# Kernel optimization log

Measured on AMD Instinct MI355X. Metric: run time of the kernel, lower is better.

The kernel has to match this reference:

```python
import jax, jax.numpy as jnp
import numpy as np

EPS_ATTN = 1e-6
EPS_LN = 1e-5  # torch nn.LayerNorm default eps
NHEAD = 8
L, D, DFF, S, B = 4, 512, 1024, 4096, 8


def _layernorm(x, g, b):
    m = jnp.mean(x, axis=-1, keepdims=True)
    v = jnp.mean((x - m) ** 2, axis=-1, keepdims=True)
    return (x - m) * jax.lax.rsqrt(v + EPS_LN) * g + b


def _layer(src, Wq, bq, Wk, bk, Wv, bv, Wo, bo, g1, be1, W1, bf1, W2, bf2, g2, be2):
    # src: (S, B, D)
    s, b, d = src.shape
    dk = d // NHEAD
    Q = (src @ Wq + bq).reshape(s, b, NHEAD, dk)
    K = (src @ Wk + bk).reshape(s, b, NHEAD, dk)
    V = (src @ Wv + bv).reshape(s, b, NHEAD, dk)
    # ELU+1 feature-map linear attention, vectorized over heads
    phiQ = jax.nn.elu(Q) + 1.0
    phiK = jax.nn.elu(K) + 1.0
    context = jnp.einsum('sbhd,sbhe->bhde', phiK, V)          # (B,H,dk,dk)
    out = jnp.einsum('sbhd,bhde->sbhe', phiQ, context)        # (S,B,H,dk)
    denom = jnp.einsum('sbhd,bhd->sbh', phiQ, phiK.sum(0))    # (S,B,H)
    out = out / (denom[..., None] + EPS_ATTN)
    attn = out.reshape(s, b, d)  # concat heads (same order as torch cat)
    out = attn @ Wo + bo
    out = _layernorm(src + out, g1, be1)
    ffn = jax.nn.relu(out @ W1 + bf1) @ W2 + bf2
    return _layernorm(out + ffn, g2, be2)


def setup_inputs() -> dict:
    key = jax.random.key(0)
    ks = jax.random.split(key, 8)
    sc = 0.02
    inp = {
        'src': jax.random.normal(ks[0], (S, B, D), jnp.float32),
        'Wq': jax.random.normal(ks[1], (L, D, D), jnp.float32) * sc,
        'bq': jnp.zeros((L, D), jnp.float32),
        'Wk': jax.random.normal(ks[2], (L, D, D), jnp.float32) * sc,
        'bk': jnp.zeros((L, D), jnp.float32),
        'Wv': jax.random.normal(ks[3], (L, D, D), jnp.float32) * sc,
        'bv': jnp.zeros((L, D), jnp.float32),
        'Wo': jax.random.normal(ks[4], (L, D, D), jnp.float32) * sc,
        'bo': jnp.zeros((L, D), jnp.float32),
        'ln1_g': jnp.ones((L, D), jnp.float32),
        'ln1_b': jnp.zeros((L, D), jnp.float32),
        'W1': jax.random.normal(ks[5], (L, D, DFF), jnp.float32) * sc,
        'b1': jnp.zeros((L, DFF), jnp.float32),
        'W2': jax.random.normal(ks[6], (L, DFF, D), jnp.float32) * sc,
        'b2': jnp.zeros((L, D), jnp.float32),
        'ln2_g': jnp.ones((L, D), jnp.float32),
        'ln2_b': jnp.zeros((L, D), jnp.float32),
    }
    return inp


def reference(src, Wq, bq, Wk, bk, Wv, bv, Wo, bo, ln1_g, ln1_b, W1, b1, W2, b2, ln2_g, ln2_b):
    x = src
    for i in range(Wq.shape[0]):  # small fixed layer count
        x = _layer(x, Wq[i], bq[i], Wk[i], bk[i], Wv[i], bv[i], Wo[i], bo[i],
                   ln1_g[i], ln1_b[i], W1[i], b1[i], W2[i], b2[i], ln2_g[i], ln2_b[i])
    return x
```

## Files before the change

kernel.cpp:

```cpp
#include <hip/hip_runtime.h>
#include <hip/hip_bf16.h>
#include <cstdint>

typedef __attribute__((ext_vector_type(8))) short short8;
typedef __attribute__((ext_vector_type(4))) float f32x4;
typedef __attribute__((ext_vector_type(4))) unsigned short ushort4v;

#define DEV static __device__ __forceinline__

DEV float bf2f(unsigned short u) {
    union { unsigned int i; float f; } v; v.i = ((unsigned int)u) << 16; return v.f;
}
DEV unsigned short f2bf(float f) {
    union { float f; unsigned int i; } v; v.f = f;
    unsigned int x = v.i;
    unsigned int r = x + 0x7fffu + ((x >> 16) & 1u);
    return (unsigned short)(r >> 16);
}

template<int EPI, int NBY, int LDA, int KT>
__global__ __launch_bounds__(256) void gemm_kernel(
    const unsigned short* __restrict__ A,
    const unsigned short* __restrict__ Bt,
    const float* __restrict__ bias,
    unsigned short* __restrict__ out1, int ldc1,
    unsigned short* __restrict__ out2)
{
    __shared__ unsigned short lds[128 * 136];
    const int t  = threadIdx.x;
    const int w  = t >> 6, l = t & 63;
    const int wr = w >> 1, wc = w & 1;
    const int lr = l & 15, lg = l >> 4;
    const int bid = blockIdx.x;
    const int j8  = bid & 7, s = bid >> 3;
    const int bx  = j8 * 32 + s / NBY;
    const int by  = s % NBY;
    const long tM = (long)bx * 128;
    const long tN = (long)by * 128;

    f32x4 acc[4][4];
#pragma unroll
    for (int i = 0; i < 4; i++)
#pragma unroll
        for (int j = 0; j < 4; j++) acc[i][j] = f32x4{0.f, 0.f, 0.f, 0.f};

    const unsigned short* ga[4];
    const unsigned short* gb[4];
    unsigned int ldsa[4], ldsb[4];
#pragma unroll
    for (int j = 0; j < 4; j++) {
        int c = (w * 4 + j) * 64 + l;
        int row = c >> 3, sc = (c & 7) ^ (row & 7);
        ga[j] = A + (tM + row) * LDA + sc * 8;
        gb[j] = Bt + (tN + row) * (long)KT + sc * 8;
        ldsa[j] = (w * 4 + j) * 512;
        ldsb[j] = 8192 + (w * 4 + j) * 512;
    }

#pragma unroll
    for (int kt = 0; kt < KT; kt += 64) {
#pragma unroll
        for (int j = 0; j < 4; j++)
            __builtin_amdgcn_global_load_lds(
                (const __attribute__((address_space(1))) void*)(ga[j] + kt),
                (__attribute__((address_space(3))) void*)(lds + ldsa[j]), 16, 0, 0);
#pragma unroll
        for (int j = 0; j < 4; j++)
            __builtin_amdgcn_global_load_lds(
                (const __attribute__((address_space(1))) void*)(gb[j] + kt),
                (__attribute__((address_space(3))) void*)(lds + ldsb[j]), 16, 0, 0);
        __syncthreads();
#pragma unroll
        for (int kk = 0; kk < 2; kk++) {
            short8 af[4], bfv[4];
#pragma unroll
            for (int mi = 0; mi < 4; mi++) {
                int r  = wr * 64 + mi * 16 + lr;
                int kc = kk * 4 + lg;
                af[mi] = *(const short8*)&lds[r * 64 + ((kc ^ (r & 7)) << 3)];
            }
#pragma unroll
            for (int ni = 0; ni < 4; ni++) {
                int n  = wc * 64 + ni * 16 + lr;
                int kc = kk * 4 + lg;
                bfv[ni] = *(const short8*)&lds[8192 + n * 64 + ((kc ^ (n & 7)) << 3)];
            }
#pragma unroll
            for (int mi = 0; mi < 4; mi++)
#pragma unroll
                for (int ni = 0; ni < 4; ni++)
                    acc[mi][ni] = __builtin_amdgcn_mfma_f32_16x16x32_bf16(
                        af[mi], bfv[ni], acc[mi][ni], 0, 0, 0);
        }
        __syncthreads();
    }

    float bv[4];
#pragma unroll
    for (int ni = 0; ni < 4; ni++) bv[ni] = bias[tN + wc * 64 + ni * 16 + lr];
    const bool doElu = (EPI == 0) && (tN < 512 || tN >= 1024);

#pragma unroll
    for (int mi = 0; mi < 4; mi++)
#pragma unroll
        for (int ni = 0; ni < 4; ni++)
#pragma unroll
            for (int j = 0; j < 4; j++) {
                float v = acc[mi][ni][j] + bv[ni];
                if (EPI == 0) { if (doElu) v = (v > 0.f) ? (v + 1.f) : expf(v); }
                if (EPI == 2) v = fmaxf(v, 0.f);
                int r = wr * 64 + mi * 16 + lg * 4 + j;
                int c = wc * 64 + ni * 16 + lr;
                lds[r * 136 + c] = f2bf(v);
            }
    __syncthreads();
    const bool toQ = (NBY == 12) && (tN >= 1024);
    unsigned short* o = toQ ? out2 : out1;
    const long ldc   = toQ ? 512 : ldc1;
    const long cb    = toQ ? (tN - 1024) : tN;
#pragma unroll
    for (int i = 0; i < 8; i++) {
        int q = i * 256 + t;
        int r = q >> 4, cc = q & 15;
        short8 v8 = *(const short8*)&lds[r * 136 + cc * 8];
        *(short8*)&o[(tM + r) * ldc + cb + cc * 8] = v8;
    }
}

template<int RESBF, int WRITEOF, int KT>
__global__ __launch_bounds__(512) void gemm_ln_kernel(
    const unsigned short* __restrict__ A, int lda,
    const unsigned short* __restrict__ Bt,
    const float* __restrict__ bias,
    const void* __restrict__ resp,
    const float* __restrict__ g,
    const float* __restrict__ be,
    float* __restrict__ of,
    unsigned short* __restrict__ ob,
    int unused)
{
    __shared__ unsigned short sA[2][128 * 32];
    __shared__ unsigned short sB[2][512 * 32];
    float* redb  = (float*)&sA[0][0];
    float* statb = redb + 1024;
    unsigned short* bb16 = (unsigned short*)&sB[0][0];
    const int t = threadIdx.x, w = t >> 6, l = t & 63, lr = l & 15, lg = l >> 4;
    const int wr = w >> 2, wc = w & 3;
    const long tM = (long)blockIdx.x * 128;

    f32x4 acc[4][8];
#pragma unroll
    for (int i = 0; i < 4; i++)
#pragma unroll
        for (int j = 0; j < 8; j++) acc[i][j] = f32x4{0.f, 0.f, 0.f, 0.f};

    const unsigned short* gA;
    const unsigned short* gB[4];
    unsigned int la, lb[4];
    {
        int c = t, row = c >> 2, sc = (c & 3) ^ ((row >> 1) & 3);
        gA = A + (tM + row) * (long)lda + sc * 8;
        la = (w * 64) * 8;
    }
#pragma unroll
    for (int j = 0; j < 4; j++) {
        int c = j * 512 + t, row = c >> 2, sc = (c & 3) ^ ((row >> 1) & 3);
        gB[j] = Bt + (long)row * KT + sc * 8;
        lb[j] = (j * 512 + w * 64) * 8;
    }

    auto STAGE = [&](int buf, int kt) {
        __builtin_amdgcn_global_load_lds(
            (const __attribute__((address_space(1))) void*)(gA + kt),
            (__attribute__((address_space(3))) void*)(&sA[buf][la]), 16, 0, 0);
#pragma unroll
        for (int j = 0; j < 4; j++)
            __builtin_amdgcn_global_load_lds(
                (const __attribute__((address_space(1))) void*)(gB[j] + kt),
                (__attribute__((address_space(3))) void*)(&sB[buf][lb[j]]), 16, 0, 0);
    };

    auto COMPUTE = [&](int buf) {
        short8 av[4], bw[8];
#pragma unroll
        for (int mi = 0; mi < 4; mi++) {
            int r = wr * 64 + mi * 16 + lr;
            av[mi] = *(const short8*)&sA[buf][r * 32 + ((lg ^ ((r >> 1) & 3)) << 3)];
        }
#pragma unroll
        for (int ni = 0; ni < 8; ni++) {
            int n = wc * 128 + ni * 16 + lr;
            bw[ni] = *(const short8*)&sB[buf][n * 32 + ((lg ^ ((n >> 1) & 3)) << 3)];
        }
#pragma unroll
        for (int mi = 0; mi < 4; mi++)
#pragma unroll
            for (int ni = 0; ni < 8; ni++)
                acc[mi][ni] = __builtin_amdgcn_mfma_f32_16x16x32_bf16(
                    av[mi], bw[ni], acc[mi][ni], 0, 0, 0);
    };

    STAGE(0, 0);
    STAGE(1, 32);
#pragma unroll
    for (int kt = 0; kt < KT; kt += 32) {
        if (kt < KT - 32) asm volatile("s_waitcnt vmcnt(5)" ::: "memory");
        else              asm volatile("s_waitcnt vmcnt(0)" ::: "memory");
        __builtin_amdgcn_s_barrier();
        COMPUTE((kt >> 5) & 1);
        asm volatile("s_waitcnt lgkmcnt(0)" ::: "memory");
        __builtin_amdgcn_s_barrier();
        if (kt + 64 < KT) STAGE((kt >> 5) & 1, kt + 64);
    }

    const float* resf = (const float*)resp;
    const unsigned short* resb = (const unsigned short*)resp;
    float gv[8], bev[8], bb[8];
#pragma unroll
    for (int ni = 0; ni < 8; ni++) {
        int col = wc * 128 + ni * 16 + lr;
        gv[ni] = g[col]; bev[ni] = be[col]; bb[ni] = bias[col];
    }
#pragma unroll
    for (int mi = 0; mi < 4; mi++)
#pragma unroll
        for (int jj = 0; jj < 4; jj++) {
            long row = tM + wr * 64 + mi * 16 + lg * 4 + jj;
#pragma unroll
            for (int ni = 0; ni < 8; ni++) {
                int col = wc * 128 + ni * 16 + lr;
                float rv = RESBF ? bf2f(resb[row * 512 + col]) : resf[row * 512 + col];
                acc[mi][ni][jj] += bb[ni] + rv;
            }
        }
    float s2[4][4], ss2[4][4];
#pragma unroll
    for (int mi = 0; mi < 4; mi++)
#pragma unroll
        for (int jj = 0; jj < 4; jj++) {
            float s = 0.f, ss = 0.f;
#pragma unroll
            for (int ni = 0; ni < 8; ni++) {
                float v = acc[mi][ni][jj];
                s += v; ss += v * v;
            }
#pragma unroll
            for (int off = 1; off < 16; off <<= 1) {
                s  += __shfl_xor(s, off);
                ss += __shfl_xor(ss, off);
            }
            s2[mi][jj] = s; ss2[mi][jj] = ss;
        }
    __syncthreads();
    if (lr == 0) {
#pragma unroll
        for (int mi = 0; mi < 4; mi++)
#pragma unroll
            for (int jj = 0; jj < 4; jj++) {
                int rb = wr * 64 + mi * 16 + lg * 4 + jj;
                redb[0 * 512 + wc * 128 + rb] = s2[mi][jj];
                redb[1 * 512 + wc * 128 + rb] = ss2[mi][jj];
            }
    }
    __syncthreads();
    if (t < 128) {
        float S  = redb[t] + redb[128 + t] + redb[256 + t] + redb[384 + t];
        float SS = redb[512 + t] + redb[640 + t] + redb[768 + t] + redb[896 + t];
        float mean = S * (1.0f / 512.0f);
        float var  = SS * (1.0f / 512.0f) - mean * mean;
        statb[t] = mean;
        statb[128 + t] = rsqrtf(fmaxf(var, 0.f) + 1e-5f);
    }
    __syncthreads();
#pragma unroll
    for (int h = 0; h < 2; h++) {
        if (wr == h) {
#pragma unroll
            for (int mi = 0; mi < 4; mi++)
#pragma unroll
                for (int jj = 0; jj < 4; jj++) {
                    int rb  = mi * 16 + lg * 4 + jj;
                    int rbg = h * 64 + rb;
                    long row = tM + rbg;
                    float mean = statb[rbg], rstd = statb[128 + rbg];
#pragma unroll
                    for (int ni = 0; ni < 8; ni++) {
                        int col = wc * 128 + ni * 16 + lr;
                        float y = (acc[mi][ni][jj] - mean) * rstd * gv[ni] + bev[ni];
                        if (WRITEOF) of[row * 512 + col] = y;
                        bb16[rb * 512 + (col ^ ((rb & 7) << 3))] = f2bf(y);
                    }
                }
        }
        __syncthreads();
#pragma unroll
        for (int i = 0; i < 8; i++) {
            int q = i * 512 + t;
            int r = q >> 6, cc = q & 63;
            short8 v8 = *(const short8*)&bb16[r * 512 + ((cc ^ (r & 7)) << 3)];
            *(short8*)&ob[(tM + h * 64 + r) * 512 + cc * 8] = v8;
        }
        __syncthreads();
    }
}

__global__ __launch_bounds__(256) void ctx_partial_kernel(
    const unsigned short* __restrict__ kv, float* __restrict__ part,
    float* __restrict__ part2)
{
    const int p = blockIdx.x, ch = blockIdx.y;
    const int b = p >> 3, h = p & 7;
    __shared__ float kb[64 * 68];
    __shared__ float vbuf[64 * 68];
    const int t = threadIdx.x;
    const int dq = t >> 4, eq = t & 15;
    f32x4 acc[4];
    f32x4 ks = {0.f, 0.f, 0.f, 0.f};
#pragma unroll
    for (int i = 0; i < 4; i++) acc[i] = f32x4{0.f, 0.f, 0.f, 0.f};

    for (int sub = 0; sub < 8; sub++) {
        int sbase = ch * 512 + sub * 64;
#pragma unroll
        for (int i = 0; i < 2; i++) {
            int idx = i * 256 + t;
            int row = idx >> 3, c8 = idx & 7;
            long ga = ((long)(sbase + row) * 8 + b) * 1024 + h * 64 + c8 * 8;
            short8 kvv = *(const short8*)&kv[ga];
            short8 vv  = *(const short8*)&kv[ga + 512];
#pragma unroll
            for (int j = 0; j < 8; j++) {
                kb[row * 68 + c8 * 8 + j]   = bf2f((unsigned short)kvv[j]);
                vbuf[row * 68 + c8 * 8 + j] = bf2f((unsigned short)vv[j]);
            }
        }
        __syncthreads();
        for (int s = 0; s < 64; s++) {
            f32x4 k4 = *(const f32x4*)&kb[s * 68 + dq * 4];
            f32x4 v4 = *(const f32x4*)&vbuf[s * 68 + eq * 4];
#pragma unroll
            for (int i = 0; i < 4; i++) acc[i] += k4[i] * v4;
            ks += k4;
        }
        __syncthreads();
    }
    float* o = part + (long)(p * 8 + ch) * 4096;
#pragma unroll
    for (int i = 0; i < 4; i++)
        *(f32x4*)&o[(dq * 4 + i) * 64 + eq * 4] = acc[i];
    if (eq == 0)
        *(f32x4*)&part2[(p * 8 + ch) * 64 + dq * 4] = ks;
}

__global__ __launch_bounds__(256) void ctx_reduce_kernel(
    const float* __restrict__ part, const float* __restrict__ part2,
    unsigned short* __restrict__ ctxA)
{
    int o = (blockIdx.x * 256 + threadIdx.x) * 4;
    int p = o >> 12, d = (o >> 6) & 63, e0 = o & 63;
    f32x4 s = {0.f, 0.f, 0.f, 0.f};
    for (int ch = 0; ch < 8; ch++)
        s += *(const f32x4*)&part[(long)(p * 8 + ch) * 4096 + d * 64 + e0];
#pragma unroll
    for (int j = 0; j < 4; j++) ctxA[p * 5120 + (e0 + j) * 64 + d] = f2bf(s[j]);
    if (e0 == 0) {
        float ksv = 0.f;
#pragma unroll
        for (int ch = 0; ch < 8; ch++) ksv += part2[(p * 8 + ch) * 64 + d];
        ctxA[p * 5120 + 4096 + d] = f2bf(ksv);
#pragma unroll
        for (int j = 1; j < 16; j++) ctxA[p * 5120 + 4096 + j * 64 + d] = 0;
    }
}

__global__ __launch_bounds__(256) void attn_out_kernel(
    unsigned short* __restrict__ kv,
    const unsigned short* __restrict__ qbuf,
    const unsigned short* __restrict__ ctxA)
{
    __shared__ unsigned short abuf[256 * 68];
    const int p = blockIdx.x;
    const int b = p >> 3, h = p & 7;
    const int t = threadIdx.x, w = t >> 6, l = t & 63, lr = l & 15, lg = l >> 4;
    const int s0 = blockIdx.y * 256 + w * 64;
    f32x4 acc[4][5];
#pragma unroll
    for (int i = 0; i < 4; i++)
#pragma unroll
        for (int j = 0; j < 5; j++) acc[i][j] = f32x4{0.f, 0.f, 0.f, 0.f};
    const unsigned short* cb = ctxA + p * 5120;
#pragma unroll
    for (int kk = 0; kk < 2; kk++) {
        short8 af[4], bfv[5];
#pragma unroll
        for (int mi = 0; mi < 4; mi++) {
            int s = s0 + mi * 16 + lr;
            af[mi] = *(const short8*)&qbuf[((long)s * 8 + b) * 512 + h * 64 + kk * 32 + lg * 8];
        }
#pragma unroll
        for (int ni = 0; ni < 5; ni++)
            bfv[ni] = *(const short8*)&cb[(ni * 16 + lr) * 64 + kk * 32 + lg * 8];
#pragma unroll
        for (int mi = 0; mi < 4; mi++)
#pragma unroll
            for (int ni = 0; ni < 5; ni++)
                acc[mi][ni] = __builtin_amdgcn_mfma_f32_16x16x32_bf16(
                    af[mi], bfv[ni], acc[mi][ni], 0, 0, 0);
    }
#pragma unroll
    for (int mi = 0; mi < 4; mi++) {
#pragma unroll
        for (int j = 0; j < 4; j++) {
            float den = __shfl(acc[mi][4][j], (l & 48));
            float rc  = 1.0f / (den + 1e-6f);
            int rloc = w * 64 + mi * 16 + lg * 4 + j;
#pragma unroll
            for (int ni = 0; ni < 4; ni++)
                abuf[rloc * 68 + ni * 16 + lr] = f2bf(acc[mi][ni][j] * rc);
        }
    }
    __syncthreads();
    const int by256 = blockIdx.y * 256;
#pragma unroll
    for (int i = 0; i < 8; i++) {
        int q = i * 256 + t;
        int r = q >> 3, c8 = q & 7;
        short8 v8 = *(const short8*)&abuf[r * 68 + c8 * 8];
        long base = ((long)(by256 + r) * 8 + b) * 1024 + h * 64;
        *(short8*)&kv[base + c8 * 8] = v8;
    }
}

__global__ __launch_bounds__(256) void cvtbf_kernel(
    const float* __restrict__ x, unsigned short* __restrict__ y)
{
    long i = ((long)blockIdx.x * 256 + threadIdx.x) * 8;
    f32x4 a = *(const f32x4*)&x[i];
    f32x4 c = *(const f32x4*)&x[i + 4];
    short8 pk;
#pragma unroll
    for (int j = 0; j < 4; j++) { pk[j] = (short)f2bf(a[j]); pk[4 + j] = (short)f2bf(c[j]); }
    *(short8*)&y[i] = pk;
}

__global__ __launch_bounds__(256) void bcat_kernel(
    const float* __restrict__ bk, const float* __restrict__ bv,
    const float* __restrict__ bq, float* __restrict__ dst)
{
    int lyr = blockIdx.x;
    int j = blockIdx.y * 256 + threadIdx.x;
    float v;
    if (j < 512)       v = bk[lyr * 512 + j];
    else if (j < 1024) v = bv[lyr * 512 + j - 512];
    else               v = bq[lyr * 512 + j - 1024];
    dst[lyr * 1536 + j] = v;
}

__global__ __launch_bounds__(256) void wconv_kernel(
    const float* __restrict__ W, unsigned short* __restrict__ Wt, int K, int N,
    long lstrW, long lstrT)
{
    __shared__ float tile[64 * 65];
    const long lz = blockIdx.z;
    const float* Wl = W + lz * lstrW;
    unsigned short* Wtl = Wt + lz * lstrT;
    const int k0 = blockIdx.x * 64, n0 = blockIdx.y * 64;
    const int t = threadIdx.x;
#pragma unroll
    for (int i = 0; i < 4; i++) {
        int q = i * 256 + t;
        int r = q >> 4, c4 = q & 15;
        f32x4 v = *(const f32x4*)&Wl[(long)(k0 + r) * N + n0 + c4 * 4];
#pragma unroll
        for (int j = 0; j < 4; j++) tile[r * 65 + c4 * 4 + j] = v[j];
    }
    __syncthreads();
#pragma unroll
    for (int i = 0; i < 4; i++) {
        int q = i * 256 + t;
        int nr = q >> 4, kc = q & 15;
        ushort4v pk;
#pragma unroll
        for (int j = 0; j < 4; j++) pk[j] = f2bf(tile[(kc * 4 + j) * 65 + nr]);
        *(ushort4v*)&Wtl[(long)(n0 + nr) * K + k0 + kc * 4] = pk;
    }
}

extern "C" void kernel_launch(void* const* d_in, const int* in_sizes, int n_in,
                              void* d_out, int out_size, void* d_ws, size_t ws_size,
                              hipStream_t stream)
{
    const float* src  = (const float*)d_in[0];
    const float* Wq   = (const float*)d_in[1];
    const float* bq   = (const float*)d_in[2];
    const float* Wk   = (const float*)d_in[3];
    const float* bk   = (const float*)d_in[4];
    const float* Wv   = (const float*)d_in[5];
    const float* bv   = (const float*)d_in[6];
    const float* Wo   = (const float*)d_in[7];
    const float* bo   = (const float*)d_in[8];
    const float* l1g  = (const float*)d_in[9];
    const float* l1b  = (const float*)d_in[10];
    const float* W1   = (const float*)d_in[11];
    const float* b1   = (const float*)d_in[12];
    const float* W2   = (const float*)d_in[13];
    const float* b2   = (const float*)d_in[14];
    const float* l2g  = (const float*)d_in[15];
    const float* l2b  = (const float*)d_in[16];

    char* ws = (char*)d_ws;
    constexpr size_t SZ_WKVQ = (size_t)4 * 1536 * 512 * 2;
    constexpr size_t SZ_WO   = (size_t)4 * 512 * 512 * 2;
    constexpr size_t SZ_W1   = (size_t)4 * 512 * 1024 * 2;
    constexpr size_t SZ_W2   = SZ_W1;
    constexpr size_t SZ_BKVQ = (size_t)4 * 1536 * 4;
    constexpr size_t SZ_R1   = (size_t)32768 * 512 * 2;
    constexpr size_t SZ_KV   = (size_t)32768 * 1024 * 2;
    constexpr size_t OFF_WKVQ = 0;
    constexpr size_t OFF_WO   = OFF_WKVQ + SZ_WKVQ;
    constexpr size_t OFF_W1   = OFF_WO + SZ_WO;
    constexpr size_t OFF_W2   = OFF_W1 + SZ_W1;
    constexpr size_t OFF_BKVQ = OFF_W2 + SZ_W2;
    constexpr size_t OFF_R1   = OFF_BKVQ + SZ_BKVQ;
    constexpr size_t OFF_KV   = OFF_R1 + SZ_R1;
    constexpr size_t OFF_KSP  = OFF_KV + SZ_KV;
    constexpr size_t OFF_CTP  = OFF_KSP + (size_t)16 * 4096 * 4;
    constexpr size_t OFF_CTA  = OFF_CTP + (size_t)64 * 8 * 4096 * 4;

    unsigned short* WKVQ = (unsigned short*)(ws + OFF_WKVQ);
    unsigned short* WOT  = (unsigned short*)(ws + OFF_WO);
    unsigned short* W1T  = (unsigned short*)(ws + OFF_W1);
    unsigned short* W2T  = (unsigned short*)(ws + OFF_W2);
    float*          BKVQ = (float*)(ws + OFF_BKVQ);
    unsigned short* R1   = (unsigned short*)(ws + OFF_R1);
    unsigned short* KV   = (unsigned short*)(ws + OFF_KV);
    float*          KSP  = (float*)(ws + OFF_KSP);
    float*          CTP  = (float*)(ws + OFF_CTP);
    unsigned short* CTA  = (unsigned short*)(ws + OFF_CTA);
    float*          F1   = (float*)d_out;
    unsigned short* QBUF = (unsigned short*)d_out;

    dim3 blk(256);
    wconv_kernel<<<dim3(8, 8, 4),  blk, 0, stream>>>(Wk, WKVQ,             512, 512, 512*512, 1536*512);
    wconv_kernel<<<dim3(8, 8, 4),  blk, 0, stream>>>(Wv, WKVQ + 512*512,   512, 512, 512*512, 1536*512);
    wconv_kernel<<<dim3(8, 8, 4),  blk, 0, stream>>>(Wq, WKVQ + 1024*512,  512, 512, 512*512, 1536*512);
    wconv_kernel<<<dim3(8, 8, 4),  blk, 0, stream>>>(Wo, WOT,              512, 512, 512*512, 512*512);
    wconv_kernel<<<dim3(8, 16, 4), blk, 0, stream>>>(W1, W1T,              512, 1024, 512*1024, 512*1024);
    wconv_kernel<<<dim3(16, 8, 4), blk, 0, stream>>>(W2, W2T,              1024, 512, 1024*512, 1024*512);
    bcat_kernel<<<dim3(4, 6), blk, 0, stream>>>(bk, bv, bq, BKVQ);
    cvtbf_kernel<<<8192, blk, 0, stream>>>(src, R1);

    for (int lyr = 0; lyr < 4; lyr++) {
        const unsigned short* wkvq = WKVQ + (size_t)lyr * 1536 * 512;
        const unsigned short* wot  = WOT  + (size_t)lyr * 512 * 512;
        const unsigned short* w1t  = W1T  + (size_t)lyr * 512 * 1024;
        const unsigned short* w2t  = W2T  + (size_t)lyr * 1024 * 512;

        gemm_kernel<0, 12, 512, 512><<<3072, blk, 0, stream>>>(R1, wkvq, BKVQ + lyr * 1536,
                                                               KV, 1024, QBUF);

        ctx_partial_kernel<<<dim3(64, 8), blk, 0, stream>>>(KV, CTP, KSP);
        ctx_reduce_kernel<<<256, blk, 0, stream>>>(CTP, KSP, CTA);

        attn_out_kernel<<<dim3(64, 16), blk, 0, stream>>>(KV, QBUF, CTA);

        if (lyr == 0)
            gemm_ln_kernel<0, 0, 512><<<256, dim3(512), 0, stream>>>(KV, 1024, wot, bo + lyr * 512, src,
                                                                     l1g + lyr * 512, l1b + lyr * 512,
                                                                     F1, R1, 0);
        else
            gemm_ln_kernel<1, 0, 512><<<256, dim3(512), 0, stream>>>(KV, 1024, wot, bo + lyr * 512, R1,
                                                                     l1g + lyr * 512, l1b + lyr * 512,
                                                                     F1, R1, 0);
        gemm_kernel<2, 8, 512, 512><<<2048, blk, 0, stream>>>(R1, w1t, b1 + lyr * 1024,
                                                              KV, 1024, nullptr);
        if (lyr == 3)
            gemm_ln_kernel<1, 1, 1024><<<256, dim3(512), 0, stream>>>(KV, 1024, w2t, b2 + lyr * 512, R1,
                                                                      l2g + lyr * 512, l2b + lyr * 512,
                                                                      F1, R1, 0);
        else
            gemm_ln_kernel<1, 0, 1024><<<256, dim3(512), 0, stream>>>(KV, 1024, w2t, b2 + lyr * 512, R1,
                                                                      l2g + lyr * 512, l2b + lyr * 512,
                                                                      F1, R1, 0);
    }
}
```

Before: 1.127 ms.

## Enlarge GEMM tile to 256x128 with 512-thread blocks sharing B tile

The generic bf16 GEMM now uses 512-thread blocks covering 256 rows by 128 columns, so each B tile loaded into LDS is reused by twice as many rows. Grid sizes are halved to match. The epilogue stages output through LDS in two 128-row halves to fit the shared buffer, which adds extra barriers. The change cuts global B traffic and block count, at the cost of more LDS and registers per block and possibly lower occupancy.

```diff
diff --git a/kernel.cpp b/kernel.cpp
--- a/kernel.cpp
+++ b/kernel.cpp
@@ -19,23 +19,23 @@
 }
 
 template<int EPI, int NBY, int LDA, int KT>
-__global__ __launch_bounds__(256) void gemm_kernel(
+__global__ __launch_bounds__(512) void gemm_kernel(
     const unsigned short* __restrict__ A,
     const unsigned short* __restrict__ Bt,
     const float* __restrict__ bias,
     unsigned short* __restrict__ out1, int ldc1,
     unsigned short* __restrict__ out2)
 {
-    __shared__ unsigned short lds[128 * 136];
+    __shared__ unsigned short lds[24576];
     const int t  = threadIdx.x;
     const int w  = t >> 6, l = t & 63;
     const int wr = w >> 1, wc = w & 1;
     const int lr = l & 15, lg = l >> 4;
     const int bid = blockIdx.x;
     const int j8  = bid & 7, s = bid >> 3;
-    const int bx  = j8 * 32 + s / NBY;
+    const int bx  = j8 * 16 + s / NBY;
     const int by  = s % NBY;
-    const long tM = (long)bx * 128;
+    const long tM = (long)bx * 256;
     const long tN = (long)by * 128;
 
     f32x4 acc[4][4];
@@ -45,16 +45,18 @@
         for (int j = 0; j < 4; j++) acc[i][j] = f32x4{0.f, 0.f, 0.f, 0.f};
 
     const unsigned short* ga[4];
-    const unsigned short* gb[4];
-    unsigned int ldsa[4], ldsb[4];
+    const unsigned short* gb[2];
 #pragma unroll
     for (int j = 0; j < 4; j++) {
-        int c = (w * 4 + j) * 64 + l;
+        int c = j * 512 + t;
         int row = c >> 3, sc = (c & 7) ^ (row & 7);
         ga[j] = A + (tM + row) * LDA + sc * 8;
+    }
+#pragma unroll
+    for (int j = 0; j < 2; j++) {
+        int c = j * 512 + t;
+        int row = c >> 3, sc = (c & 7) ^ (row & 7);
         gb[j] = Bt + (tN + row) * (long)KT + sc * 8;
-        ldsa[j] = (w * 4 + j) * 512;
-        ldsb[j] = 8192 + (w * 4 + j) * 512;
     }
 
 #pragma unroll
@@ -63,12 +65,12 @@
         for (int j = 0; j < 4; j++)
             __builtin_amdgcn_global_load_lds(
                 (const __attribute__((address_space(1))) void*)(ga[j] + kt),
-                (__attribute__((address_space(3))) void*)(lds + ldsa[j]), 16, 0, 0);
-#pragma unroll
-        for (int j = 0; j < 4; j++)
+                (__attribute__((address_space(3))) void*)(lds + (j * 512 + (t & ~63)) * 8), 16, 0, 0);
+#pragma unroll
+        for (int j = 0; j < 2; j++)
             __builtin_amdgcn_global_load_lds(
                 (const __attribute__((address_space(1))) void*)(gb[j] + kt),
-                (__attribute__((address_space(3))) void*)(lds + ldsb[j]), 16, 0, 0);
+                (__attribute__((address_space(3))) void*)(lds + 16384 + (j * 512 + (t & ~63)) * 8), 16, 0, 0);
         __syncthreads();
 #pragma unroll
         for (int kk = 0; kk < 2; kk++) {
@@ -83,7 +85,7 @@
             for (int ni = 0; ni < 4; ni++) {
                 int n  = wc * 64 + ni * 16 + lr;
                 int kc = kk * 4 + lg;
-                bfv[ni] = *(const short8*)&lds[8192 + n * 64 + ((kc ^ (n & 7)) << 3)];
+                bfv[ni] = *(const short8*)&lds[16384 + n * 64 + ((kc ^ (n & 7)) << 3)];
             }
 #pragma unroll
             for (int mi = 0; mi < 4; mi++)
@@ -100,30 +102,37 @@
     for (int ni = 0; ni < 4; ni++) bv[ni] = bias[tN + wc * 64 + ni * 16 + lr];
     const bool doElu = (EPI == 0) && (tN < 512 || tN >= 1024);
 
-#pragma unroll
-    for (int mi = 0; mi < 4; mi++)
-#pragma unroll
-        for (int ni = 0; ni < 4; ni++)
-#pragma unroll
-            for (int j = 0; j < 4; j++) {
-                float v = acc[mi][ni][j] + bv[ni];
-                if (EPI == 0) { if (doElu) v = (v > 0.f) ? (v + 1.f) : expf(v); }
-                if (EPI == 2) v = fmaxf(v, 0.f);
-                int r = wr * 64 + mi * 16 + lg * 4 + j;
-                int c = wc * 64 + ni * 16 + lr;
-                lds[r * 136 + c] = f2bf(v);
-            }
-    __syncthreads();
     const bool toQ = (NBY == 12) && (tN >= 1024);
     unsigned short* o = toQ ? out2 : out1;
     const long ldc   = toQ ? 512 : ldc1;
     const long cb    = toQ ? (tN - 1024) : tN;
-#pragma unroll
-    for (int i = 0; i < 8; i++) {
-        int q = i * 256 + t;
-        int r = q >> 4, cc = q & 15;
-        short8 v8 = *(const short8*)&lds[r * 136 + cc * 8];
-        *(short8*)&o[(tM + r) * ldc + cb + cc * 8] = v8;
+
+#pragma unroll
+    for (int h = 0; h < 2; h++) {
+        if ((wr >> 1) == h) {
+#pragma unroll
+            for (int mi = 0; mi < 4; mi++)
+#pragma unroll
+                for (int ni = 0; ni < 4; ni++)
+#pragma unroll
+                    for (int j = 0; j < 4; j++) {
+                        float v = acc[mi][ni][j] + bv[ni];
+                        if (EPI == 0) { if (doElu) v = (v > 0.f) ? (v + 1.f) : expf(v); }
+                        if (EPI == 2) v = fmaxf(v, 0.f);
+                        int r = (wr & 1) * 64 + mi * 16 + lg * 4 + j;
+                        int c = wc * 64 + ni * 16 + lr;
+                        lds[r * 136 + c] = f2bf(v);
+                    }
+        }
+        __syncthreads();
+#pragma unroll
+        for (int i = 0; i < 4; i++) {
+            int q = i * 512 + t;
+            int r = q >> 4, cc = q & 15;
+            short8 v8 = *(const short8*)&lds[r * 136 + cc * 8];
+            *(short8*)&o[(tM + h * 128 + r) * ldc + cb + cc * 8] = v8;
+        }
+        __syncthreads();
     }
 }
 
@@ -556,8 +565,8 @@
         const unsigned short* w1t  = W1T  + (size_t)lyr * 512 * 1024;
         const unsigned short* w2t  = W2T  + (size_t)lyr * 1024 * 512;
 
-        gemm_kernel<0, 12, 512, 512><<<3072, blk, 0, stream>>>(R1, wkvq, BKVQ + lyr * 1536,
-                                                               KV, 1024, QBUF);
+        gemm_kernel<0, 12, 512, 512><<<1536, dim3(512), 0, stream>>>(R1, wkvq, BKVQ + lyr * 1536,
+                                                                     KV, 1024, QBUF);
 
         ctx_partial_kernel<<<dim3(64, 8), blk, 0, stream>>>(KV, CTP, KSP);
         ctx_reduce_kernel<<<256, blk, 0, stream>>>(CTP, KSP, CTA);
@@ -572,8 +581,8 @@
             gemm_ln_kernel<1, 0, 512><<<256, dim3(512), 0, stream>>>(KV, 1024, wot, bo + lyr * 512, R1,
                                                                      l1g + lyr * 512, l1b + lyr * 512,
                                                                      F1, R1, 0);
-        gemm_kernel<2, 8, 512, 512><<<2048, blk, 0, stream>>>(R1, w1t, b1 + lyr * 1024,
-                                                              KV, 1024, nullptr);
+        gemm_kernel<2, 8, 512, 512><<<1024, dim3(512), 0, stream>>>(R1, w1t, b1 + lyr * 1024,
+                                                                    KV, 1024, nullptr);
         if (lyr == 3)
             gemm_ln_kernel<1, 1, 1024><<<256, dim3(512), 0, stream>>>(KV, 1024, w2t, b2 + lyr * 512, R1,
                                                                       l2g + lyr * 512, l2b + lyr * 512,
```

New measurement: 1.199 ms. 1.06x slower.
